# Performance work log

Measured on AMD Instinct MI355X. Metric: run time of the kernel, lower is better.

## Reference

```python
import jax, jax.numpy as jnp
import numpy as np

BATCH = 2048
N_MOL = 16
HEADS = 8      # C
A_DIM = 64     # embedding_dim
B_DIM = 64     # output_dim
D_IN = 64
POS_DIM = 6
CA = HEADS * A_DIM
CB = HEADS * B_DIM


def _pos_encoding(n_mol):
    # get_pos_encoding_(pos, C=6, dim_embedding=3): 3 sin + 3 cos terms
    def enc(p):
        return np.array([np.sin(p / 6.0 ** (2 * i / 3.0)) for i in (1, 2, 3)]
                        + [np.cos(p / 6.0 ** (2 * i / 3.0)) for i in (1, 2, 3)])
    return np.stack([enc(i) for i in range(n_mol)]).astype(np.float32)  # (n_mol, 6)


def setup_inputs() -> dict:
    key = jax.random.key(0)
    ks = jax.random.split(key, 8)
    d_ext = D_IN + POS_DIM

    def w(k, fi, fo):
        return jax.random.normal(k, (fi, fo), jnp.float32) / np.sqrt(fi).astype(np.float32)

    return {
        "x": jax.random.normal(ks[0], (BATCH, N_MOL, D_IN), jnp.float32),
        "flow_mask": jnp.ones((N_MOL,), jnp.float32),
        "Wk_h": w(ks[1], d_ext, CA), "bk_h": jnp.zeros((CA,), jnp.float32),
        "Wk_o": w(ks[2], CA, CA),    "bk_o": jnp.zeros((CA,), jnp.float32),
        "Wq_h": w(ks[3], d_ext, CA), "bq_h": jnp.zeros((CA,), jnp.float32),
        "Wq_o": w(ks[4], CA, CA),    "bq_o": jnp.zeros((CA,), jnp.float32),
        "Wv_h": w(ks[5], d_ext, CB), "bv_h": jnp.zeros((CB,), jnp.float32),
        "Wv_o": w(ks[6], CB, CB),    "bv_o": jnp.zeros((CB,), jnp.float32),
        "pos_emb": jnp.asarray(_pos_encoding(N_MOL)),
    }


def reference(x, flow_mask, Wk_h, bk_h, Wk_o, bk_o, Wq_h, bq_h, Wq_o, bq_o,
              Wv_h, bv_h, Wv_o, bv_o, pos_emb):
    batch = x.shape[0]
    # one_hot_extend_: append positional encoding per molecule -> (b, n_mol, d_in+6)
    xe = jnp.concatenate(
        [x, jnp.broadcast_to(pos_emb[None], (batch, N_MOL, POS_DIM))], axis=-1)

    def mlp(Wh, bh, Wo, bo):  # 1 silu hidden layer + linear output
        return jax.nn.silu(xe @ Wh + bh) @ Wo + bo

    k = mlp(Wk_h, bk_h, Wk_o, bk_o).reshape(batch, N_MOL, HEADS, A_DIM)
    q = mlp(Wq_h, bq_h, Wq_o, bq_o).reshape(batch, N_MOL, HEADS, A_DIM)
    v = mlp(Wv_h, bv_h, Wv_o, bv_o).reshape(batch, N_MOL, HEADS, B_DIM)

    norm = 1.0 / np.sqrt(A_DIM).astype(np.float32)
    # scores over molecule pairs, per head: (b, i, j, c)
    arg = jnp.einsum('i,j,bica,bjca->bijc', flow_mask, flow_mask, k, q) * norm
    w = jax.nn.softplus(arg) + 1e-5
    mask_self = 1.0 - jnp.eye(N_MOL, dtype=x.dtype)  # mask_self=True, n_mol>1
    w = w * mask_self[None, :, :, None]
    w = w / jnp.sum(w, axis=-2, keepdims=True)  # normalize over j
    # weighted combine, summing over j and heads c -> (b, n_mol, B)
    return jnp.einsum('j,bijc,bjcd->bid', flow_mask, w, v)
```

## Files before the change

### kernel.cpp

```cpp
#include <hip/hip_runtime.h>
#include <hip/hip_bf16.h>

typedef __hip_bfloat16 bf16;
typedef __attribute__((ext_vector_type(8))) short bf16x8;
typedef __attribute__((ext_vector_type(4))) float floatx4;
typedef unsigned short ushort;
typedef unsigned int uint;

#define ROWS 32768
#define KX 96

#define MFMA(a, b, c) __builtin_amdgcn_mfma_f32_16x16x32_bf16(a, b, c, 0, 0, 0)
#define GL_LDS(gp, lp) __builtin_amdgcn_global_load_lds( \
    (const __attribute__((address_space(1))) unsigned int*)(gp), \
    (__attribute__((address_space(3))) unsigned int*)(lp), 16, 0, 0)

__device__ __forceinline__ ushort f2bf(float f) {
  union { float f; unsigned int i; } u; u.f = f;
  return (ushort)((u.i + 0x7fffu + ((u.i >> 16) & 1u)) >> 16);
}

__global__ void prep_misc(const float* __restrict__ x, const float* __restrict__ pos,
    const float* __restrict__ bk1, const float* __restrict__ bq1, const float* __restrict__ bv1,
    const float* __restrict__ bk2, const float* __restrict__ bq2, const float* __restrict__ bv2,
    bf16* __restrict__ xe, float* __restrict__ b1, float* __restrict__ b2)
{
  int idx = blockIdx.x * 256 + threadIdx.x;
  if (idx < ROWS * KX) {
    int r = idx / KX, col = idx - r * KX;
    float v = 0.f;
    if (col < 64)      v = x[r * 64 + col];
    else if (col < 70) v = pos[(r & 15) * 6 + (col - 64)];
    xe[idx] = __float2bfloat16(v);
  } else if (idx < ROWS * KX + 3072) {
    int i = idx - ROWS * KX;
    if (i < 1536) {
      int z = i >> 9, nl = i & 511;
      const float* s = (z == 0) ? bk1 : (z == 1) ? bq1 : bv1;
      b1[i] = s[nl];
    } else {
      int j = i - 1536;
      int z = j >> 9, nl = j & 511;
      const float* s = (z == 0) ? bk2 : (z == 1) ? bq2 : bv2;
      b2[j] = s[nl];
    }
  }
}

__global__ __launch_bounds__(256) void prep_wt(
    const float* __restrict__ Wk_h, const float* __restrict__ Wq_h, const float* __restrict__ Wv_h,
    const float* __restrict__ Wk_o, const float* __restrict__ Wq_o, const float* __restrict__ Wv_o,
    bf16* __restrict__ w1t, bf16* __restrict__ w2t)
{
  __shared__ float tile[32][33];
  const int bid = blockIdx.x;
  const int c = threadIdx.x & 31, r0 = threadIdx.x >> 5;
  if (bid < 768) {
    const int z = bid >> 8, rem = bid & 255;
    const int nt = rem >> 4, kt = rem & 15;
    const float* src = (z == 0) ? Wk_o : (z == 1) ? Wq_o : Wv_o;
    #pragma unroll
    for (int rr = 0; rr < 4; ++rr) {
      int r = r0 + rr * 8;
      tile[r][c] = src[(kt * 32 + r) * 512 + nt * 32 + c];
    }
    __syncthreads();
    #pragma unroll
    for (int rr = 0; rr < 4; ++rr) {
      int r = r0 + rr * 8;
      w2t[((long)z * 512 + nt * 32 + r) * 512 + kt * 32 + c] = __float2bfloat16(tile[c][r]);
    }
  } else {
    const int b2i = bid - 768;
    const int z = b2i / 48, rem = b2i - z * 48;
    const int kt = rem >> 4, nt = rem & 15;
    const float* src = (z == 0) ? Wk_h : (z == 1) ? Wq_h : Wv_h;
    #pragma unroll
    for (int rr = 0; rr < 4; ++rr) {
      int r = r0 + rr * 8;
      int k = kt * 32 + r;
      tile[r][c] = (k < 70) ? src[k * 512 + nt * 32 + c] : 0.f;
    }
    __syncthreads();
    #pragma unroll
    for (int rr = 0; rr < 4; ++rr) {
      int r = r0 + rr * 8;
      w1t[((long)z * 512 + nt * 32 + r) * KX + kt * 32 + c] = __float2bfloat16(tile[c][r]);
    }
  }
}

__global__ __launch_bounds__(256, 3) void gemm1_reg(
    const bf16* __restrict__ xe, const bf16* __restrict__ w1t,
    const float* __restrict__ bias, bf16* __restrict__ hid)
{
  const int tid = threadIdx.x, w = tid >> 6, lane = tid & 63;
  const int r0 = blockIdx.x * 64;
  const int bn = blockIdx.y * 256;
  const int rowl = lane & 15, kg = (lane >> 4) * 8;

  bf16x8 a0, a1, a2;
  {
    const bf16* xp = xe + (long)(r0 + 16 * w + rowl) * KX + kg;
    a0 = *(const bf16x8*)xp;
    a1 = *(const bf16x8*)(xp + 32);
    a2 = *(const bf16x8*)(xp + 64);
  }

  floatx4 acc[16];
  #pragma unroll
  for (int nt = 0; nt < 16; ++nt) acc[nt] = (floatx4){0.f, 0.f, 0.f, 0.f};

  const bf16* wp = w1t + (long)(bn + rowl) * KX + kg;
  #pragma unroll
  for (int nt = 0; nt < 16; ++nt) {
    const bf16* bp = wp + (long)nt * 16 * KX;
    bf16x8 b0 = *(const bf16x8*)bp;
    bf16x8 b1 = *(const bf16x8*)(bp + 32);
    bf16x8 b2 = *(const bf16x8*)(bp + 64);
    acc[nt] = MFMA(a0, b0, acc[nt]);
    acc[nt] = MFMA(a1, b1, acc[nt]);
    acc[nt] = MFMA(a2, b2, acc[nt]);
  }

  const int m0 = r0 + 16 * w + (lane >> 4) * 4;
  #pragma unroll
  for (int nt = 0; nt < 16; ++nt) {
    const int col = bn + nt * 16 + rowl;
    const float bv = bias[col];
    #pragma unroll
    for (int r = 0; r < 4; ++r) {
      float v = acc[nt][r] + bv;
      v = v / (1.f + __expf(-v));
      float vp = __shfl_xor(v, 1);
      if (!(rowl & 1)) {
        uint pk = (uint)f2bf(v) | ((uint)f2bf(vp) << 16);
        *(uint*)(hid + (long)(m0 + r) * 1536 + col) = pk;
      }
    }
  }
}

__global__ __launch_bounds__(256) void mlp_gemm2(
    const bf16* __restrict__ A,
    const bf16* __restrict__ Bt,
    const float* __restrict__ bias,
    bf16* __restrict__ C)
{
  __shared__ __align__(16) bf16 As[2][128 * 32];
  __shared__ __align__(16) bf16 Bs[2][128 * 32];
  const int tid  = threadIdx.x;
  const int wave = tid >> 6, lane = tid & 63;
  const int z  = blockIdx.y >> 2;
  const int bn = (blockIdx.y & 3) * 128;
  const int bm = blockIdx.x * 128;
  const int bnf = z * 512 + bn;
  const bf16* Ap  = A + z * 512;
  const bf16* Btp = Bt + (long)z * 512 * 512;
  const int wm = (wave >> 1) * 64;
  const int wn = (wave & 1) * 64;
  const int arow = lane >> 2;
  const int acol = (lane & 3) * 8;

#define STAGE2(buf, t) do {                                                   \
    const int k0_ = (t) * 32;                                                 \
    _Pragma("unroll")                                                         \
    for (int ch = 0; ch < 2; ++ch) {                                          \
      const int rb = wave * 32 + ch * 16;                                     \
      GL_LDS(Ap  + (long)(bm + rb + arow) * 1536 + k0_ + acol, As[buf] + rb * 32); \
      GL_LDS(Btp + (long)(bn + rb + arow) * 512  + k0_ + acol, Bs[buf] + rb * 32); \
    } } while (0)

  STAGE2(0, 0);
  asm volatile("s_waitcnt vmcnt(0)" ::: "memory");
  __syncthreads();

  floatx4 acc[4][4] = {};
  int cur = 0;
  for (int t = 0; t < 16; ++t) {
    if (t + 1 < 16) STAGE2(cur ^ 1, t + 1);
    bf16x8 af[4], bfr[4];
    #pragma unroll
    for (int mi = 0; mi < 4; ++mi)
      af[mi] = *(const bf16x8*)(As[cur] + (wm + mi * 16 + (lane & 15)) * 32 + (lane >> 4) * 8);
    #pragma unroll
    for (int ni = 0; ni < 4; ++ni)
      bfr[ni] = *(const bf16x8*)(Bs[cur] + (wn + ni * 16 + (lane & 15)) * 32 + (lane >> 4) * 8);
    #pragma unroll
    for (int mi = 0; mi < 4; ++mi)
      #pragma unroll
      for (int ni = 0; ni < 4; ++ni)
        acc[mi][ni] = MFMA(af[mi], bfr[ni], acc[mi][ni]);
    if (t + 1 < 16) {
      asm volatile("s_waitcnt vmcnt(0)" ::: "memory");
      __syncthreads();
      cur ^= 1;
    }
  }
#undef STAGE2

  if (z < 2) {
    bf16* Cz = C + (long)z * ROWS * 512;
    #pragma unroll
    for (int mi = 0; mi < 4; ++mi) {
      #pragma unroll
      for (int ni = 0; ni < 4; ++ni) {
        const int ncf = bnf + wn + ni * 16 + (lane & 15);
        const int nc  = ncf & 511;
        const float bv = bias[ncf];
        #pragma unroll
        for (int r = 0; r < 4; ++r) {
          const long m = bm + wm + mi * 16 + (lane >> 4) * 4 + r;
          Cz[m * 512 + nc] = __float2bfloat16(acc[mi][ni][r] + bv);
        }
      }
    }
  } else {
    ushort* vt = (ushort*)C + (long)2 * ROWS * 512;
    #pragma unroll
    for (int mi = 0; mi < 4; ++mi) {
      const int m0 = bm + wm + mi * 16;
      const long bb = (long)(m0 >> 4) * 8192;
      #pragma unroll
      for (int ni = 0; ni < 4; ++ni) {
        const int ncf = bnf + wn + ni * 16 + (lane & 15);
        const int nc  = ncf & 511;
        const float bv = bias[ncf];
        float v0 = acc[mi][ni][0] + bv, v1 = acc[mi][ni][1] + bv;
        float v2 = acc[mi][ni][2] + bv, v3 = acc[mi][ni][3] + bv;
        uint2 pk;
        pk.x = (uint)f2bf(v0) | ((uint)f2bf(v1) << 16);
        pk.y = (uint)f2bf(v2) | ((uint)f2bf(v3) << 16);
        *(uint2*)(vt + bb + (long)nc * 16 + (lane >> 4) * 4) = pk;
      }
    }
  }
}

__global__ __launch_bounds__(256) void attn_v3(
    const bf16* __restrict__ kqv,
    const float* __restrict__ flow_mask,
    float* __restrict__ out)
{
  __shared__ ushort wn_s[4 * 16 * 40];
  __shared__ float  fm_s[16];

  const int tid  = threadIdx.x;
  const int lane = tid & 63;
  const int wave = tid >> 6;
  const int b    = blockIdx.x;

  if (tid < 16) fm_s[tid] = flow_mask[tid];
  __syncthreads();

  const int jcol = lane & 15;
  const int rgrp = lane >> 4;
  const int ko   = rgrp * 8;

  {
    const bf16* kg = kqv + ((long)b * 16 + jcol) * 512;
    const bf16* qg = kg + 16777216;
    const float fmj = fm_s[jcol];
    #pragma unroll
    for (int h = 0; h < 2; ++h) {
      const int c = wave + h * 4;
      floatx4 acc = {0.f, 0.f, 0.f, 0.f};
      bf16x8 a0 = *(const bf16x8*)(kg + c * 64 + ko);
      bf16x8 a1 = *(const bf16x8*)(kg + c * 64 + 32 + ko);
      bf16x8 b0 = *(const bf16x8*)(qg + c * 64 + ko);
      bf16x8 b1 = *(const bf16x8*)(qg + c * 64 + 32 + ko);
      acc = MFMA(a0, b0, acc);
      acc = MFMA(a1, b1, acc);

      float wv[4], ss[4];
      #pragma unroll
      for (int r = 0; r < 4; ++r) {
        const int i = rgrp * 4 + r;
        float arg = acc[r] * (fm_s[i] * fmj * 0.125f);
        float sp  = fmaxf(arg, 0.f) + log1pf(__expf(-fabsf(arg)));
        float wvv = sp + 1e-5f;
        if (i == jcol) wvv = 0.f;
        wv[r] = wvv; ss[r] = wvv;
      }
      #pragma unroll
      for (int m = 1; m < 16; m <<= 1) {
        #pragma unroll
        for (int r = 0; r < 4; ++r) ss[r] += __shfl_xor(ss[r], m);
      }
      const int hp = c >> 1, chl = c & 1;
      #pragma unroll
      for (int r = 0; r < 4; ++r) {
        const int i = rgrp * 4 + r;
        wn_s[hp * 640 + i * 40 + chl * 16 + jcol] = f2bf(wv[r] / ss[r] * fmj);
      }
    }
  }
  __syncthreads();

  {
    const int dcol = wave * 16 + jcol;
    const ushort* vb = (const ushort*)kqv + (long)2 * ROWS * 512 + (long)b * 8192;
    floatx4 o = {0.f, 0.f, 0.f, 0.f};
    #pragma unroll
    for (int hp = 0; hp < 4; ++hp) {
      bf16x8 af = *(const bf16x8*)&wn_s[hp * 640 + jcol * 40 + ko];
      const int c  = 2 * hp + (ko >> 4);
      const int jb = ko & 15;
      bf16x8 bfr = *(const bf16x8*)(vb + (long)(c * 64 + dcol) * 16 + jb);
      o = MFMA(af, bfr, o);
    }
    float* ob = out + (long)b * 1024 + dcol;
    #pragma unroll
    for (int r = 0; r < 4; ++r) ob[(rgrp * 4 + r) * 64] = o[r];
  }
}

extern "C" void kernel_launch(void* const* d_in, const int* in_sizes, int n_in,
                              void* d_out, int out_size, void* d_ws, size_t ws_size,
                              hipStream_t stream) {
  const float* x    = (const float*)d_in[0];
  const float* fmk  = (const float*)d_in[1];
  const float* Wk_h = (const float*)d_in[2];
  const float* bk_h = (const float*)d_in[3];
  const float* Wk_o = (const float*)d_in[4];
  const float* bk_o = (const float*)d_in[5];
  const float* Wq_h = (const float*)d_in[6];
  const float* bq_h = (const float*)d_in[7];
  const float* Wq_o = (const float*)d_in[8];
  const float* bq_o = (const float*)d_in[9];
  const float* Wv_h = (const float*)d_in[10];
  const float* bv_h = (const float*)d_in[11];
  const float* Wv_o = (const float*)d_in[12];
  const float* bv_o = (const float*)d_in[13];
  const float* pos  = (const float*)d_in[14];
  float* out = (float*)d_out;

  char* ws = (char*)d_ws;
  bf16*  xe  = (bf16*)(ws + 0);
  bf16*  w1t = (bf16*)(ws + 6291456);
  bf16*  w2t = (bf16*)(ws + 6586368);
  float* b1  = (float*)(ws + 8159232);
  float* b2  = (float*)(ws + 8165376);
  bf16*  hid = (bf16*)(ws + 8171520);
  bf16*  kqv = (bf16*)(ws + 108834816);
  if (ws_size < 209498112ULL) return;

  prep_misc<<<12300, 256, 0, stream>>>(x, pos, bk_h, bq_h, bv_h, bk_o, bq_o, bv_o,
                                       xe, b1, b2);
  prep_wt<<<912, 256, 0, stream>>>(Wk_h, Wq_h, Wv_h, Wk_o, Wq_o, Wv_o, w1t, w2t);
  gemm1_reg<<<dim3(512, 6), 256, 0, stream>>>(xe, w1t, b1, hid);
  mlp_gemm2<<<dim3(256, 12), 256, 0, stream>>>(hid, w2t, b2, kqv);
  attn_v3<<<2048, 256, 0, stream>>>(kqv, fmk, out);
}
```

Before: 262.4 us.

## Stage GEMM tiles through LDS with multi-buffered async loads and counted waits

The first MLP GEMM switches from direct register loads over a 64x256 tile to a 128x128 LDS-tiled kernel. It issues all three K slices up front with global_load_lds and waits on partial vmcnt counts, so MFMA work on early slices overlaps the loads of later ones. The second GEMM moves from a double buffer to a four-slot ring with three stages in flight and partial vmcnt waits, instead of draining all loads every iteration. This uses more LDS per block, which may cut occupancy. The gemm1 epilogue also drops the paired packed store in favour of scalar bf16 stores.

```diff
diff --git a/kernel.cpp b/kernel.cpp
--- a/kernel.cpp
+++ b/kernel.cpp
@@ -90,65 +90,77 @@
   }
 }
 
-__global__ __launch_bounds__(256, 3) void gemm1_reg(
+__global__ __launch_bounds__(256) void gemm1_pf(
     const bf16* __restrict__ xe, const bf16* __restrict__ w1t,
     const float* __restrict__ bias, bf16* __restrict__ hid)
 {
-  const int tid = threadIdx.x, w = tid >> 6, lane = tid & 63;
-  const int r0 = blockIdx.x * 64;
-  const int bn = blockIdx.y * 256;
-  const int rowl = lane & 15, kg = (lane >> 4) * 8;
-
-  bf16x8 a0, a1, a2;
-  {
-    const bf16* xp = xe + (long)(r0 + 16 * w + rowl) * KX + kg;
-    a0 = *(const bf16x8*)xp;
-    a1 = *(const bf16x8*)(xp + 32);
-    a2 = *(const bf16x8*)(xp + 64);
-  }
-
-  floatx4 acc[16];
+  __shared__ __align__(16) bf16 As[3][128 * 32];
+  __shared__ __align__(16) bf16 Bs[3][128 * 32];
+  const int tid  = threadIdx.x;
+  const int wave = tid >> 6, lane = tid & 63;
+  const int bm  = blockIdx.x * 128;
+  const int bnf = blockIdx.y * 128;
+  const int wm = (wave >> 1) * 64;
+  const int wn = (wave & 1) * 64;
+  const int arow = lane >> 2;
+  const int acol = (lane & 3) * 8;
+
   #pragma unroll
-  for (int nt = 0; nt < 16; ++nt) acc[nt] = (floatx4){0.f, 0.f, 0.f, 0.f};
-
-  const bf16* wp = w1t + (long)(bn + rowl) * KX + kg;
+  for (int s = 0; s < 3; ++s) {
+    const int k0 = s * 32;
+    #pragma unroll
+    for (int ch = 0; ch < 2; ++ch) {
+      const int rb = wave * 32 + ch * 16;
+      GL_LDS(xe  + (long)(bm  + rb + arow) * KX + k0 + acol, As[s] + rb * 32);
+      GL_LDS(w1t + (long)(bnf + rb + arow) * KX + k0 + acol, Bs[s] + rb * 32);
+    }
+  }
+
+  floatx4 acc[4][4] = {};
   #pragma unroll
-  for (int nt = 0; nt < 16; ++nt) {
-    const bf16* bp = wp + (long)nt * 16 * KX;
-    bf16x8 b0 = *(const bf16x8*)bp;
-    bf16x8 b1 = *(const bf16x8*)(bp + 32);
-    bf16x8 b2 = *(const bf16x8*)(bp + 64);
-    acc[nt] = MFMA(a0, b0, acc[nt]);
-    acc[nt] = MFMA(a1, b1, acc[nt]);
-    acc[nt] = MFMA(a2, b2, acc[nt]);
-  }
-
-  const int m0 = r0 + 16 * w + (lane >> 4) * 4;
+  for (int s = 0; s < 3; ++s) {
+    if (s == 0)      asm volatile("s_waitcnt vmcnt(8)\n\ts_barrier" ::: "memory");
+    else if (s == 1) asm volatile("s_waitcnt vmcnt(4)\n\ts_barrier" ::: "memory");
+    else             asm volatile("s_waitcnt vmcnt(0)\n\ts_barrier" ::: "memory");
+    bf16x8 af[4], bfr[4];
+    #pragma unroll
+    for (int mi = 0; mi < 4; ++mi)
+      af[mi] = *(const bf16x8*)(As[s] + (wm + mi * 16 + (lane & 15)) * 32 + (lane >> 4) * 8);
+    #pragma unroll
+    for (int ni = 0; ni < 4; ++ni)
+      bfr[ni] = *(const bf16x8*)(Bs[s] + (wn + ni * 16 + (lane & 15)) * 32 + (lane >> 4) * 8);
+    #pragma unroll
+    for (int mi = 0; mi < 4; ++mi)
+      #pragma unroll
+      for (int ni = 0; ni < 4; ++ni)
+        acc[mi][ni] = MFMA(af[mi], bfr[ni], acc[mi][ni]);
+  }
+
   #pragma unroll
-  for (int nt = 0; nt < 16; ++nt) {
-    const int col = bn + nt * 16 + rowl;
-    const float bv = bias[col];
-    #pragma unroll
-    for (int r = 0; r < 4; ++r) {
-      float v = acc[nt][r] + bv;
-      v = v / (1.f + __expf(-v));
-      float vp = __shfl_xor(v, 1);
-      if (!(rowl & 1)) {
-        uint pk = (uint)f2bf(v) | ((uint)f2bf(vp) << 16);
-        *(uint*)(hid + (long)(m0 + r) * 1536 + col) = pk;
-      }
-    }
-  }
-}
-
-__global__ __launch_bounds__(256) void mlp_gemm2(
+  for (int mi = 0; mi < 4; ++mi) {
+    #pragma unroll
+    for (int ni = 0; ni < 4; ++ni) {
+      const int nc = bnf + wn + ni * 16 + (lane & 15);
+      const float bv = bias[nc];
+      #pragma unroll
+      for (int r = 0; r < 4; ++r) {
+        const long m = bm + wm + mi * 16 + (lane >> 4) * 4 + r;
+        float v = acc[mi][ni][r] + bv;
+        v = v / (1.f + __expf(-v));
+        hid[m * 1536 + nc] = __float2bfloat16(v);
+      }
+    }
+  }
+}
+
+__global__ __launch_bounds__(256) void gemm2_cnt(
     const bf16* __restrict__ A,
     const bf16* __restrict__ Bt,
     const float* __restrict__ bias,
     bf16* __restrict__ C)
 {
-  __shared__ __align__(16) bf16 As[2][128 * 32];
-  __shared__ __align__(16) bf16 Bs[2][128 * 32];
+  __shared__ __align__(16) bf16 As[4][128 * 32];
+  __shared__ __align__(16) bf16 Bs[4][128 * 32];
   const int tid  = threadIdx.x;
   const int wave = tid >> 6, lane = tid & 63;
   const int z  = blockIdx.y >> 2;
@@ -162,40 +174,40 @@
   const int arow = lane >> 2;
   const int acol = (lane & 3) * 8;
 
-#define STAGE2(buf, t) do {                                                   \
-    const int k0_ = (t) * 32;                                                 \
-    _Pragma("unroll")                                                         \
-    for (int ch = 0; ch < 2; ++ch) {                                          \
-      const int rb = wave * 32 + ch * 16;                                     \
+#define STAGE2(buf, t) do {                                                        \
+    const int k0_ = (t) * 32;                                                      \
+    _Pragma("unroll")                                                              \
+    for (int ch = 0; ch < 2; ++ch) {                                               \
+      const int rb = wave * 32 + ch * 16;                                          \
       GL_LDS(Ap  + (long)(bm + rb + arow) * 1536 + k0_ + acol, As[buf] + rb * 32); \
       GL_LDS(Btp + (long)(bn + rb + arow) * 512  + k0_ + acol, Bs[buf] + rb * 32); \
     } } while (0)
 
   STAGE2(0, 0);
-  asm volatile("s_waitcnt vmcnt(0)" ::: "memory");
-  __syncthreads();
+  STAGE2(1, 1);
+  STAGE2(2, 2);
 
   floatx4 acc[4][4] = {};
-  int cur = 0;
   for (int t = 0; t < 16; ++t) {
-    if (t + 1 < 16) STAGE2(cur ^ 1, t + 1);
+    if (t <= 13)      asm volatile("s_waitcnt vmcnt(8)\n\ts_barrier" ::: "memory");
+    else if (t == 14) asm volatile("s_waitcnt vmcnt(4)\n\ts_barrier" ::: "memory");
+    else              asm volatile("s_waitcnt vmcnt(0)\n\ts_barrier" ::: "memory");
+    if (t + 3 < 16) STAGE2((t + 3) & 3, t + 3);
+
+    const bf16* Ab = As[t & 3];
+    const bf16* Bb = Bs[t & 3];
     bf16x8 af[4], bfr[4];
     #pragma unroll
     for (int mi = 0; mi < 4; ++mi)
-      af[mi] = *(const bf16x8*)(As[cur] + (wm + mi * 16 + (lane & 15)) * 32 + (lane >> 4) * 8);
+      af[mi] = *(const bf16x8*)(Ab + (wm + mi * 16 + (lane & 15)) * 32 + (lane >> 4) * 8);
     #pragma unroll
     for (int ni = 0; ni < 4; ++ni)
-      bfr[ni] = *(const bf16x8*)(Bs[cur] + (wn + ni * 16 + (lane & 15)) * 32 + (lane >> 4) * 8);
+      bfr[ni] = *(const bf16x8*)(Bb + (wn + ni * 16 + (lane & 15)) * 32 + (lane >> 4) * 8);
     #pragma unroll
     for (int mi = 0; mi < 4; ++mi)
       #pragma unroll
       for (int ni = 0; ni < 4; ++ni)
         acc[mi][ni] = MFMA(af[mi], bfr[ni], acc[mi][ni]);
-    if (t + 1 < 16) {
-      asm volatile("s_waitcnt vmcnt(0)" ::: "memory");
-      __syncthreads();
-      cur ^= 1;
-    }
   }
 #undef STAGE2
 
@@ -348,7 +360,7 @@
   prep_misc<<<12300, 256, 0, stream>>>(x, pos, bk_h, bq_h, bv_h, bk_o, bq_o, bv_o,
                                        xe, b1, b2);
   prep_wt<<<912, 256, 0, stream>>>(Wk_h, Wq_h, Wv_h, Wk_o, Wq_o, Wv_o, w1t, w2t);
-  gemm1_reg<<<dim3(512, 6), 256, 0, stream>>>(xe, w1t, b1, hid);
-  mlp_gemm2<<<dim3(256, 12), 256, 0, stream>>>(hid, w2t, b2, kqv);
+  gemm1_pf<<<dim3(256, 12), 256, 0, stream>>>(xe, w1t, b1, hid);
+  gemm2_cnt<<<dim3(256, 12), 256, 0, stream>>>(hid, w2t, b2, kqv);
   attn_v3<<<2048, 256, 0, stream>>>(kqv, fmk, out);
 }
```

Measured after the change: 231.3 us. -11.9%, faster.
